# Optimization experiments

Measured on AMD Instinct MI355X. Metric: run time of the kernel, lower is better.

Reference implementation:

```python
import jax, jax.numpy as jnp
import numpy as np
import math


def custom_round(x):
    # floor(x - sign(x)*tiny + 0.5): consistent tie-breaking at .5 boundaries
    tiny = jnp.finfo(x.dtype).eps
    return jnp.floor(x - jnp.sign(x) * tiny + 0.5)


def g_x(x):
    # f(x) with the coordinate of largest rounding error pushed to the
    # next-nearest integer (parity-flip candidate). x: [N, d]
    f = custom_round(x)
    delta = jnp.abs(x - f)
    k = jnp.argmax(delta, axis=-1)                      # [N]
    mask = jax.nn.one_hot(k, x.shape[-1], dtype=jnp.bool_)  # [N, d]
    # direction of the flip, matching the original branchy logic:
    #   x>=0: +1 if f < x else -1 ; x<0: +1 if f <= x else -1
    up = jnp.where(x >= 0, f < x, f <= x)
    adj = f + jnp.where(up, 1.0, -1.0).astype(x.dtype)
    return jnp.where(mask, adj, f)


def closest_point_Dn(x):
    f = custom_round(x)
    even = (jnp.mod(jnp.sum(f, axis=-1), 2.0) == 0.0)[:, None]
    return jnp.where(even, f, g_x(x))


def closest_point_E8(x):
    # E8 = D8 union (D8 + 1/2): take the better of the two cosets
    y0 = closest_point_Dn(x)
    y1 = closest_point_Dn(x - 0.5) + 0.5
    d0 = jnp.sum((x - y0) ** 2, axis=-1, keepdims=True)
    d1 = jnp.sum((x - y1) ** 2, axis=-1, keepdims=True)
    return jnp.where(d0 < d1, y0, y1)


def make_tie_dither(d=8):
    irr = np.sqrt(np.array([2, 3, 5, 7, 11, 13, 17, 19][:d], dtype=np.float32))
    u = irr - np.floor(irr) - 0.5
    u = u / np.linalg.norm(u)
    delta = (2.0 ** -40) * 0.5
    return jnp.asarray(delta * u, dtype=jnp.float32)


def setup_inputs() -> dict:
    key = jax.random.key(0)
    kx, _ = jax.random.split(key)
    N, d = 4_000_000, 8
    x = jax.random.normal(kx, (N, d), dtype=jnp.float32) * 2.0
    beta = jnp.array(1.0, dtype=jnp.float32)
    eps = make_tie_dither(d)
    return {"x": x, "beta": beta, "eps": eps}


def reference(x, beta, eps):
    # Lattice quantization with learnable scale and tie dither:
    # y = beta * Q_E8(x / beta + eps)
    z = x / beta + eps[None, :]
    q = closest_point_E8(z)
    return beta * q
```

## Files before the change

### kernel.cpp

```cpp
#include <hip/hip_runtime.h>

#pragma clang fp contract(off)

#define TINY_EPS 1.1920928955078125e-07f

typedef float f4 __attribute__((ext_vector_type(4)));

__device__ __forceinline__ void dn8(const float z[8], float out[8]) {
    float f[8], delta[8];
    int par = 0;
#pragma unroll
    for (int j = 0; j < 8; ++j) {
        float x  = z[j];
        float t  = x - __builtin_copysignf(TINY_EPS, x);
        float fv = floorf(t + 0.5f);
        f[j]     = fv;
        delta[j] = fabsf(x - fv);
        par += (int)fv;
    }
    int   k  = 0;
    float bd = delta[0], xk = z[0], fk = f[0];
#pragma unroll
    for (int j = 1; j < 8; ++j) {
        bool better = delta[j] > bd;
        bd = better ? delta[j] : bd;
        xk = better ? z[j] : xk;
        fk = better ? f[j] : fk;
        k  = better ? j : k;
    }
    bool  up  = (xk >= 0.0f) ? (fk < xk) : (fk <= xk);
    float adj = fk + (up ? 1.0f : -1.0f);
    bool  odd = (par & 1) != 0;
#pragma unroll
    for (int j = 0; j < 8; ++j)
        out[j] = (odd && (j == k)) ? adj : f[j];
}

__device__ __forceinline__ void e8_point(const float z[8], float beta, float q[8]) {
    float y0[8];
    dn8(z, y0);

    float zs[8], y1[8];
#pragma unroll
    for (int j = 0; j < 8; ++j) zs[j] = z[j] - 0.5f;
    dn8(zs, y1);
#pragma unroll
    for (int j = 0; j < 8; ++j) y1[j] = y1[j] + 0.5f;

    float d0 = 0.0f, d1 = 0.0f;
#pragma unroll
    for (int j = 0; j < 8; ++j) {
        float t0 = __fsub_rn(z[j], y0[j]);
        d0       = __fadd_rn(d0, __fmul_rn(t0, t0));
        float t1 = __fsub_rn(z[j], y1[j]);
        d1       = __fadd_rn(d1, __fmul_rn(t1, t1));
    }
    bool pick0 = d0 < d1;

#pragma unroll
    for (int j = 0; j < 8; ++j) q[j] = beta * (pick0 ? y0[j] : y1[j]);
}

__global__ void __launch_bounds__(256)
e8_quant_kernel(const float* __restrict__ x, const float* __restrict__ beta_p,
                const float* __restrict__ eps, float* __restrict__ out, int N) {
    int i = blockIdx.x * blockDim.x + threadIdx.x;
    if (i >= N) return;

    float beta = *beta_p;
    float e[8];
#pragma unroll
    for (int j = 0; j < 8; ++j) e[j] = eps[j];

    const f4* xp = reinterpret_cast<const f4*>(x) + (size_t)i * 2;
    f4 a = xp[0];
    f4 b = xp[1];
    float z[8] = {a.x, a.y, a.z, a.w, b.x, b.y, b.z, b.w};

    if (beta == 1.0f) {
#pragma unroll
        for (int j = 0; j < 8; ++j) z[j] = z[j] + e[j];
    } else {
#pragma unroll
        for (int j = 0; j < 8; ++j) z[j] = z[j] / beta + e[j];
    }

    float q[8];
    e8_point(z, beta, q);

    f4* op = reinterpret_cast<f4*>(out) + (size_t)i * 2;
    f4 s0 = {q[0], q[1], q[2], q[3]};
    f4 s1 = {q[4], q[5], q[6], q[7]};
    op[0] = s0;
    op[1] = s1;
}

extern "C" void kernel_launch(void* const* d_in, const int* in_sizes, int n_in,
                              void* d_out, int out_size, void* d_ws, size_t ws_size,
                              hipStream_t stream) {
    const float* x      = (const float*)d_in[0];
    const float* beta_p = (const float*)d_in[1];
    const float* eps    = (const float*)d_in[2];
    float*       out    = (float*)d_out;

    int N     = in_sizes[0] / 8;
    int block = 256;
    int grid  = (N + block - 1) / block;
    hipLaunchKernelGGL(e8_quant_kernel, dim3(grid), dim3(block), 0, stream,
                       x, beta_p, eps, out, N);
}
```

Before: 42.86 us.

## Reuse Dn8 rounding residuals for distances and process two points per thread

Dn8 now returns the rounded vector, per-coordinate residuals, and the flip value, without materialising both candidate points. Squared distances are built from the stored residuals, and the parity comes from a float sum. Each thread now handles two E8 points to get more loads in flight, and launch bounds request a minimum occupancy. This cuts ALU work and improves memory-level parallelism, but the memory access pattern per thread becomes strided and register use goes up.

```diff
diff --git a/kernel.cpp b/kernel.cpp
--- a/kernel.cpp
+++ b/kernel.cpp
@@ -6,93 +6,123 @@
 
 typedef float f4 __attribute__((ext_vector_type(4)));
 
-__device__ __forceinline__ void dn8(const float z[8], float out[8]) {
-    float f[8], delta[8];
-    int par = 0;
+struct Dn8 {
+    float f[8];
+    float d[8];
+    float adj;
+    float rflip;
+    int   k;
+    bool  odd;
+};
+
+__device__ __forceinline__ Dn8 dn8(const float z[8]) {
+    Dn8 r;
+    float fsum = 0.0f;
 #pragma unroll
     for (int j = 0; j < 8; ++j) {
         float x  = z[j];
         float t  = x - __builtin_copysignf(TINY_EPS, x);
         float fv = floorf(t + 0.5f);
-        f[j]     = fv;
-        delta[j] = fabsf(x - fv);
-        par += (int)fv;
+        r.f[j] = fv;
+        r.d[j] = fabsf(x - fv);
+        fsum   = __fadd_rn(fsum, fv);
     }
     int   k  = 0;
-    float bd = delta[0], xk = z[0], fk = f[0];
+    float bd = r.d[0], xk = z[0], fk = r.f[0];
 #pragma unroll
     for (int j = 1; j < 8; ++j) {
-        bool better = delta[j] > bd;
-        bd = better ? delta[j] : bd;
+        bool better = r.d[j] > bd;
+        bd = better ? r.d[j] : bd;
         xk = better ? z[j] : xk;
-        fk = better ? f[j] : fk;
+        fk = better ? r.f[j] : fk;
         k  = better ? j : k;
     }
     bool  up  = (xk >= 0.0f) ? (fk < xk) : (fk <= xk);
     float adj = fk + (up ? 1.0f : -1.0f);
-    bool  odd = (par & 1) != 0;
-#pragma unroll
-    for (int j = 0; j < 8; ++j)
-        out[j] = (odd && (j == k)) ? adj : f[j];
+    r.adj   = adj;
+    r.rflip = __fsub_rn(xk, adj);
+    r.k     = k;
+    r.odd   = (((int)fsum) & 1) != 0;
+    return r;
 }
 
 __device__ __forceinline__ void e8_point(const float z[8], float beta, float q[8]) {
-    float y0[8];
-    dn8(z, y0);
-
-    float zs[8], y1[8];
+    float zs[8];
 #pragma unroll
     for (int j = 0; j < 8; ++j) zs[j] = z[j] - 0.5f;
-    dn8(zs, y1);
-#pragma unroll
-    for (int j = 0; j < 8; ++j) y1[j] = y1[j] + 0.5f;
+
+    Dn8 A = dn8(z);
+    Dn8 B = dn8(zs);
 
     float d0 = 0.0f, d1 = 0.0f;
 #pragma unroll
     for (int j = 0; j < 8; ++j) {
-        float t0 = __fsub_rn(z[j], y0[j]);
-        d0       = __fadd_rn(d0, __fmul_rn(t0, t0));
-        float t1 = __fsub_rn(z[j], y1[j]);
-        d1       = __fadd_rn(d1, __fmul_rn(t1, t1));
+        bool  mA = A.odd && (j == A.k);
+        bool  mB = B.odd && (j == B.k);
+        float vA = mA ? A.rflip : A.d[j];
+        float vB = mB ? B.rflip : B.d[j];
+        d0 = __fadd_rn(d0, __fmul_rn(vA, vA));
+        d1 = __fadd_rn(d1, __fmul_rn(vB, vB));
     }
-    bool pick0 = d0 < d1;
-
+    bool  pick0 = d0 < d1;
+    float c     = pick0 ? 0.0f : 0.5f;
 #pragma unroll
-    for (int j = 0; j < 8; ++j) q[j] = beta * (pick0 ? y0[j] : y1[j]);
+    for (int j = 0; j < 8; ++j) {
+        bool  mA = A.odd && (j == A.k);
+        bool  mB = B.odd && (j == B.k);
+        float yA = mA ? A.adj : A.f[j];
+        float yB = mB ? B.adj : B.f[j];
+        float w  = pick0 ? yA : yB;
+        q[j] = __fmul_rn(beta, __fadd_rn(w, c));
+    }
 }
 
-__global__ void __launch_bounds__(256)
+__global__ void __launch_bounds__(256, 4)
 e8_quant_kernel(const float* __restrict__ x, const float* __restrict__ beta_p,
                 const float* __restrict__ eps, float* __restrict__ out, int N) {
-    int i = blockIdx.x * blockDim.x + threadIdx.x;
-    if (i >= N) return;
+    int i  = blockIdx.x * blockDim.x + threadIdx.x;
+    int p0 = i * 2;
+    if (p0 >= N) return;
+    bool w2  = (p0 + 1) < N;
+    int  p1c = w2 ? (p0 + 1) : p0;
 
     float beta = *beta_p;
     float e[8];
 #pragma unroll
     for (int j = 0; j < 8; ++j) e[j] = eps[j];
 
-    const f4* xp = reinterpret_cast<const f4*>(x) + (size_t)i * 2;
-    f4 a = xp[0];
-    f4 b = xp[1];
-    float z[8] = {a.x, a.y, a.z, a.w, b.x, b.y, b.z, b.w};
+    const f4* xp = reinterpret_cast<const f4*>(x);
+    f4 a0 = xp[(size_t)p0 * 2 + 0];
+    f4 a1 = xp[(size_t)p0 * 2 + 1];
+    f4 b0 = xp[(size_t)p1c * 2 + 0];
+    f4 b1 = xp[(size_t)p1c * 2 + 1];
+
+    float zA[8] = {a0.x, a0.y, a0.z, a0.w, a1.x, a1.y, a1.z, a1.w};
+    float zB[8] = {b0.x, b0.y, b0.z, b0.w, b1.x, b1.y, b1.z, b1.w};
 
     if (beta == 1.0f) {
 #pragma unroll
-        for (int j = 0; j < 8; ++j) z[j] = z[j] + e[j];
+        for (int j = 0; j < 8; ++j) { zA[j] = zA[j] + e[j]; zB[j] = zB[j] + e[j]; }
     } else {
 #pragma unroll
-        for (int j = 0; j < 8; ++j) z[j] = z[j] / beta + e[j];
+        for (int j = 0; j < 8; ++j) { zA[j] = zA[j] / beta + e[j]; zB[j] = zB[j] / beta + e[j]; }
     }
 
-    float q[8];
-    e8_point(z, beta, q);
+    float qA[8], qB[8];
+    e8_point(zA, beta, qA);
+    e8_point(zB, beta, qB);
 
-    f4* op = reinterpret_cast<f4*>(out) + (size_t)i * 2;
-    f4 s0 = {q[0], q[1], q[2], q[3]};
-    f4 s1 = {q[4], q[5], q[6], q[7]};
-    op[0] = s0;
-    op[1] = s1;
+    f4* op = reinterpret_cast<f4*>(out);
+    f4 sA0 = {qA[0], qA[1], qA[2], qA[3]};
+    f4 sA1 = {qA[4], qA[5], qA[6], qA[7]};
+    op[(size_t)p0 * 2 + 0] = sA0;
+    op[(size_t)p0 * 2 + 1] = sA1;
+    if (w2) {
+        f4 sB0 = {qB[0], qB[1], qB[2], qB[3]};
+        f4 sB1 = {qB[4], qB[5], qB[6], qB[7]};
+        op[(size_t)(p0 + 1) * 2 + 0] = sB0;
+        op[(size_t)(p0 + 1) * 2 + 1] = sB1;
+    }
 }
 
 extern "C" void kernel_launch(void* const* d_in, const int* in_sizes, int n_in,
@@ -104,8 +134,9 @@
     float*       out    = (float*)d_out;
 
     int N     = in_sizes[0] / 8;
+    int pairs = (N + 1) / 2;
     int block = 256;
-    int grid  = (N + block - 1) / block;
+    int grid  = (pairs + block - 1) / block;
     hipLaunchKernelGGL(e8_quant_kernel, dim3(grid), dim3(block), 0, stream,
                        x, beta_p, eps, out, N);
 }
```

After: 52.48 us. 22.4% more time.

## Pack both E8 cosets into float2 math and stage stores through LDS

Applied to the files above, without the earlier changes.

Computes the two D8 coset roundings together as float2 pairs (aimed at packed FP32 ops), reuses the signed residuals for both the argmax and the distance sums, and drops the separate dn8 calls. Output is written through a padded shared-memory tile so each wave issues fully contiguous 16-byte nontemporal stores instead of two strided stores per thread. The cost is shared memory, a block barrier, and a little more register pressure. The fallback path still handles partial blocks.

```diff
diff --git a/kernel.cpp b/kernel.cpp
--- a/kernel.cpp
+++ b/kernel.cpp
@@ -5,67 +5,16 @@
 #define TINY_EPS 1.1920928955078125e-07f
 
 typedef float f4 __attribute__((ext_vector_type(4)));
-
-__device__ __forceinline__ void dn8(const float z[8], float out[8]) {
-    float f[8], delta[8];
-    int par = 0;
-#pragma unroll
-    for (int j = 0; j < 8; ++j) {
-        float x  = z[j];
-        float t  = x - __builtin_copysignf(TINY_EPS, x);
-        float fv = floorf(t + 0.5f);
-        f[j]     = fv;
-        delta[j] = fabsf(x - fv);
-        par += (int)fv;
-    }
-    int   k  = 0;
-    float bd = delta[0], xk = z[0], fk = f[0];
-#pragma unroll
-    for (int j = 1; j < 8; ++j) {
-        bool better = delta[j] > bd;
-        bd = better ? delta[j] : bd;
-        xk = better ? z[j] : xk;
-        fk = better ? f[j] : fk;
-        k  = better ? j : k;
-    }
-    bool  up  = (xk >= 0.0f) ? (fk < xk) : (fk <= xk);
-    float adj = fk + (up ? 1.0f : -1.0f);
-    bool  odd = (par & 1) != 0;
-#pragma unroll
-    for (int j = 0; j < 8; ++j)
-        out[j] = (odd && (j == k)) ? adj : f[j];
-}
-
-__device__ __forceinline__ void e8_point(const float z[8], float beta, float q[8]) {
-    float y0[8];
-    dn8(z, y0);
-
-    float zs[8], y1[8];
-#pragma unroll
-    for (int j = 0; j < 8; ++j) zs[j] = z[j] - 0.5f;
-    dn8(zs, y1);
-#pragma unroll
-    for (int j = 0; j < 8; ++j) y1[j] = y1[j] + 0.5f;
-
-    float d0 = 0.0f, d1 = 0.0f;
-#pragma unroll
-    for (int j = 0; j < 8; ++j) {
-        float t0 = __fsub_rn(z[j], y0[j]);
-        d0       = __fadd_rn(d0, __fmul_rn(t0, t0));
-        float t1 = __fsub_rn(z[j], y1[j]);
-        d1       = __fadd_rn(d1, __fmul_rn(t1, t1));
-    }
-    bool pick0 = d0 < d1;
-
-#pragma unroll
-    for (int j = 0; j < 8; ++j) q[j] = beta * (pick0 ? y0[j] : y1[j]);
-}
+typedef float f2 __attribute__((ext_vector_type(2)));
 
 __global__ void __launch_bounds__(256)
 e8_quant_kernel(const float* __restrict__ x, const float* __restrict__ beta_p,
                 const float* __restrict__ eps, float* __restrict__ out, int N) {
-    int i = blockIdx.x * blockDim.x + threadIdx.x;
-    if (i >= N) return;
+    __shared__ float tile[8][257];
+    int tid = threadIdx.x;
+    int i   = blockIdx.x * 256 + tid;
+    bool full_block = ((blockIdx.x + 1) * 256) <= N;
+    if (!full_block && i >= N) return;
 
     float beta = *beta_p;
     float e[8];
@@ -85,14 +34,84 @@
         for (int j = 0; j < 8; ++j) z[j] = z[j] / beta + e[j];
     }
 
+    f2 fpk[8], dpk[8];
+    f2 fsum = {0.0f, 0.0f};
+#pragma unroll
+    for (int j = 0; j < 8; ++j) {
+        f2 xv = {z[j], z[j] - 0.5f};
+        f2 cs = {__builtin_copysignf(TINY_EPS, xv.x),
+                 __builtin_copysignf(TINY_EPS, xv.y)};
+        f2 t  = xv - cs;
+        f2 u  = t + 0.5f;
+        f2 fv = {floorf(u.x), floorf(u.y)};
+        fpk[j] = fv;
+        dpk[j] = xv - fv;
+        fsum   = fsum + fv;
+    }
+    bool oddA = (((int)fsum.x) & 1) != 0;
+    bool oddB = (((int)fsum.y) & 1) != 0;
+
+    int   kA = 0,        kB = 0;
+    float bdA = dpk[0].x, fkA = fpk[0].x;
+    float bdB = dpk[0].y, fkB = fpk[0].y;
+#pragma unroll
+    for (int j = 1; j < 8; ++j) {
+        bool bA = fabsf(dpk[j].x) > fabsf(bdA);
+        bdA = bA ? dpk[j].x : bdA;
+        fkA = bA ? fpk[j].x : fkA;
+        kA  = bA ? j : kA;
+        bool bB = fabsf(dpk[j].y) > fabsf(bdB);
+        bdB = bB ? dpk[j].y : bdB;
+        fkB = bB ? fpk[j].y : fkB;
+        kB  = bB ? j : kB;
+    }
+    bool  upA    = (fkA < 0.0f) ? (bdA >= 0.0f) : (bdA > 0.0f);
+    float adjA   = fkA + (upA ? 1.0f : -1.0f);
+    bool  upB    = (fkB < 0.0f) ? (bdB >= 0.0f) : (bdB > 0.0f);
+    float adjB05 = (fkB + (upB ? 1.0f : -1.0f)) + 0.5f;
+
+    f2 dacc = {0.0f, 0.0f};
+    float yA[8], yB[8];
+#pragma unroll
+    for (int j = 0; j < 8; ++j) {
+        bool  mA  = oddA && (j == kA);
+        bool  mB  = oddB && (j == kB);
+        float yBj = fpk[j].y + 0.5f;
+        float vA  = mA ? __fsub_rn(z[j], adjA)   : dpk[j].x;
+        float vB  = mB ? __fsub_rn(z[j], adjB05) : __fsub_rn(z[j], yBj);
+        f2 v = {vA, vB};
+        dacc = dacc + v * v;
+        yA[j] = mA ? adjA   : fpk[j].x;
+        yB[j] = mB ? adjB05 : yBj;
+    }
+    bool pick0 = dacc.x < dacc.y;
+
     float q[8];
-    e8_point(z, beta, q);
+#pragma unroll
+    for (int j = 0; j < 8; ++j)
+        q[j] = __fmul_rn(beta, pick0 ? yA[j] : yB[j]);
 
-    f4* op = reinterpret_cast<f4*>(out) + (size_t)i * 2;
-    f4 s0 = {q[0], q[1], q[2], q[3]};
-    f4 s1 = {q[4], q[5], q[6], q[7]};
-    op[0] = s0;
-    op[1] = s1;
+    if (full_block) {
+#pragma unroll
+        for (int j = 0; j < 8; ++j) tile[j][tid] = q[j];
+        __syncthreads();
+        int wave = tid >> 6, lane = tid & 63;
+        int wb   = wave << 6;
+        f4* op   = reinterpret_cast<f4*>(out) + (size_t)blockIdx.x * 512 + wave * 128;
+#pragma unroll
+        for (int c = 0; c < 2; ++c) {
+            int p = wb + c * 32 + (lane >> 1);
+            int h = (lane & 1) << 2;
+            f4 v = {tile[h + 0][p], tile[h + 1][p], tile[h + 2][p], tile[h + 3][p]};
+            __builtin_nontemporal_store(v, op + c * 64 + lane);
+        }
+    } else {
+        f4* op = reinterpret_cast<f4*>(out) + (size_t)i * 2;
+        f4 s0 = {q[0], q[1], q[2], q[3]};
+        f4 s1 = {q[4], q[5], q[6], q[7]};
+        op[0] = s0;
+        op[1] = s1;
+    }
 }
 
 extern "C" void kernel_launch(void* const* d_in, const int* in_sizes, int n_in,
```

Result: faster. 41.57 us (-3.0%).
